# Kernel tuning notes

Measured on AMD Instinct MI355X. Metric: run time of the kernel, lower is better.

The kernel has to match this reference:

```python
import jax, jax.numpy as jnp
import numpy as np

NA = 100000  # number of a-type nodes (rows of adj)
NB = 100000  # number of b-type nodes (cols of adj)
NE = 1600000 # number of edges (nnz of adj)
BF = 128     # b_features
AF = 128     # a_features


def setup_inputs() -> dict:
    key = jax.random.key(0)
    k1, k2, k3, k4, k5, k6 = jax.random.split(key, 6)
    stdv = 1.0 / np.sqrt(BF)
    return {
        "b_input": jax.random.normal(k1, (NB, BF), dtype=jnp.float32),
        "edge_rows": jax.random.randint(k2, (NE,), 0, NA, dtype=jnp.int32),
        "edge_cols": jax.random.randint(k3, (NE,), 0, NB, dtype=jnp.int32),
        "edge_vals": jax.random.uniform(k4, (NE,), dtype=jnp.float32),
        "a_weight": jax.random.uniform(k5, (BF, AF), minval=-stdv, maxval=stdv, dtype=jnp.float32),
        "a_bias": jax.random.uniform(k6, (AF,), minval=-stdv, maxval=stdv, dtype=jnp.float32),
    }


def reference(b_input, edge_rows, edge_cols, edge_vals, a_weight, a_bias):
    # a_support = b_input @ a_weight            : [NB, AF]
    a_support = jnp.matmul(b_input, a_weight)
    # a_output = spmm(adj, a_support)           : [NA, AF]
    # adj[r, c] = edge_vals at (edge_rows, edge_cols)
    gathered = a_support[edge_cols] * edge_vals[:, None]   # [NE, AF]
    a_output = jax.ops.segment_sum(gathered, edge_rows, num_segments=NA)
    # bias=True -> early return of a-side output
    return a_output + a_bias
```

## Files before the change

kernel.cpp:

```cpp
#include <hip/hip_runtime.h>
#include <hip/hip_bf16.h>

#define AF 128
#define BF 128
#define BROWS 32
#define CAP_F 800
#define SORT_CAP 1024
#define CROWS 1024
#define CAP_C 18432
#define CHUNK1 2048
#define NCOARSE_MAX 128

typedef __attribute__((ext_vector_type(8))) short bf16x8;
typedef __attribute__((ext_vector_type(4))) float f32x4;

__device__ inline unsigned short f2bf(float f) {
    unsigned int u = __float_as_uint(f);
    u += 0x7FFF + ((u >> 16) & 1);
    return (unsigned short)(u >> 16);
}
__device__ inline unsigned int pk2bf(float x, float y) {
    __hip_bfloat162 h = __float22bfloat162_rn(make_float2(x, y));
    return *(unsigned int*)&h;
}
__device__ inline float bflo(unsigned int u) { return __uint_as_float(u << 16); }
__device__ inline float bfhi(unsigned int u) { return __uint_as_float(u & 0xFFFF0000u); }

__global__ __launch_bounds__(256) void prep_kernel(const float* __restrict__ W,
                                                   unsigned short* __restrict__ Wt,
                                                   int* __restrict__ grelC,
                                                   int* __restrict__ grelF) {
    const int idx = blockIdx.x * 256 + threadIdx.x;
    const int n = idx >> 7, k = idx & 127;
    Wt[idx] = f2bf(W[(size_t)k * AF + n]);
    if (blockIdx.x == 0) {
        #pragma unroll
        for (int i = threadIdx.x; i < 1024; i += 256) grelC[i] = 0;
        #pragma unroll
        for (int i = threadIdx.x; i < 3328; i += 256) grelF[i] = 0;
    }
}

__global__ __launch_bounds__(256) void gemm_kernel(const float* __restrict__ Bin,
                                                   const unsigned short* __restrict__ Wt,
                                                   unsigned int* __restrict__ Sup, int NB) {
    const int tid = threadIdx.x;
    const int lane = tid & 63;
    const int wave = tid >> 6;
    const int row0 = blockIdx.x * 64;
    const int m = lane & 15;
    const int quad = lane >> 4;

    int arow = row0 + wave * 16 + m;
    int arow_c = (arow < NB) ? arow : (NB - 1);
    const float* ap = Bin + (size_t)arow_c * BF + quad * 8;
    bf16x8 af[4];
    #pragma unroll
    for (int ks = 0; ks < 4; ks++) {
        float4 lo = *(const float4*)(ap + ks * 32);
        float4 hi = *(const float4*)(ap + ks * 32 + 4);
        union { unsigned int u[4]; bf16x8 v; } cv;
        cv.u[0] = pk2bf(lo.x, lo.y); cv.u[1] = pk2bf(lo.z, lo.w);
        cv.u[2] = pk2bf(hi.x, hi.y); cv.u[3] = pk2bf(hi.z, hi.w);
        af[ks] = cv.v;
    }

    f32x4 acc[8];
    #pragma unroll
    for (int nt = 0; nt < 8; nt++) {
        f32x4 a = {0.f, 0.f, 0.f, 0.f};
        const unsigned short* wp = Wt + (size_t)(nt * 16 + m) * 128 + quad * 8;
        #pragma unroll
        for (int ks = 0; ks < 4; ks++) {
            bf16x8 bf = *(const bf16x8*)(wp + ks * 32);
            a = __builtin_amdgcn_mfma_f32_16x16x32_bf16(af[ks], bf, a, 0, 0, 0);
        }
        acc[nt] = a;
    }
    #pragma unroll
    for (int nt = 0; nt < 4; nt++) {
        #pragma unroll
        for (int r = 0; r < 4; r++) {
            int row = row0 + wave * 16 + quad * 4 + r;
            if (row < NB)
                Sup[(size_t)row * 64 + nt * 16 + m] = pk2bf(acc[nt][r], acc[nt + 4][r]);
        }
    }
}

__global__ __launch_bounds__(256) void binA_kernel(const int* __restrict__ rows,
                                                   const int* __restrict__ cols,
                                                   const float* __restrict__ vals,
                                                   int* __restrict__ grelC,
                                                   int2* __restrict__ binnedC,
                                                   int NE, int NCOARSE) {
    __shared__ int h[NCOARSE_MAX];
    __shared__ int rbase[NCOARSE_MAX];
    const int tid = threadIdx.x;
    int base = blockIdx.x * CHUNK1;
    int ke[8]; int px[8]; float pv[8];
    #pragma unroll
    for (int i = 0; i < 8; i++) {
        int e = base + tid + i * 256;
        if (e < NE) {
            int r = rows[e];
            ke[i] = r >> 10;
            px[i] = cols[e] | ((r & 1023) << 17);
            pv[i] = vals[e];
        } else ke[i] = -1;
    }
    if (tid < NCOARSE) h[tid] = 0;
    __syncthreads();
    #pragma unroll
    for (int i = 0; i < 8; i++)
        if (ke[i] >= 0) atomicAdd(&h[ke[i]], 1);
    __syncthreads();
    if (tid < NCOARSE) {
        int c = h[tid];
        rbase[tid] = tid * CAP_C + (c ? atomicAdd(&grelC[tid], c) : 0);
        h[tid] = 0;
    }
    __syncthreads();
    #pragma unroll
    for (int i = 0; i < 8; i++) {
        if (ke[i] >= 0) {
            int lp = atomicAdd(&h[ke[i]], 1);
            binnedC[rbase[ke[i]] + lp] = make_int2(px[i], __float_as_int(pv[i]));
        }
    }
}

__global__ __launch_bounds__(256) void passA2_kernel(const int2* __restrict__ binnedC,
                                                     const int* __restrict__ grelC,
                                                     int* __restrict__ grelF,
                                                     int2* __restrict__ binnedF, int NBUCK) {
    __shared__ int h[32];
    __shared__ int rb[32];
    const int tid = threadIdx.x;
    const int j = blockIdx.x >> 5;
    const int s = blockIdx.x & 31;
    int n = grelC[j]; if (n > CAP_C) n = CAP_C;
    const int st = (n * s) >> 5;
    const int en = (n * (s + 1)) >> 5;
    const int2* src = binnedC + (size_t)j * CAP_C;

    int sub[3]; int qx[3]; int qy[3];
    #pragma unroll
    for (int i = 0; i < 3; i++) {
        int idx = st + tid + i * 256;
        if (idx < en) {
            int2 p = src[idx];
            sub[i] = (p.x >> 22) & 31;
            qx[i] = p.x & 0x3FFFFF;
            qy[i] = p.y;
        } else sub[i] = -1;
    }
    if (tid < 32) h[tid] = 0;
    __syncthreads();
    #pragma unroll
    for (int i = 0; i < 3; i++)
        if (sub[i] >= 0) atomicAdd(&h[sub[i]], 1);
    __syncthreads();
    if (tid < 32) {
        int c = h[tid];
        int fine = j * 32 + tid;
        rb[tid] = (fine < NBUCK) ? (fine * CAP_F + (c ? atomicAdd(&grelF[fine], c) : 0)) : 0;
        h[tid] = 0;
    }
    __syncthreads();
    #pragma unroll
    for (int i = 0; i < 3; i++) {
        if (sub[i] >= 0) {
            int lp = atomicAdd(&h[sub[i]], 1);
            binnedF[(size_t)rb[sub[i]] + lp] = make_int2(qx[i], qy[i]);
        }
    }
}

__global__ __launch_bounds__(256) void spmm_sorted_kernel(const unsigned short* __restrict__ Sup,
                                                          const int2* __restrict__ binned,
                                                          const int* __restrict__ grel,
                                                          const float* __restrict__ bias,
                                                          float* __restrict__ out, int NA) {
    __shared__ int2 spxy[SORT_CAP];
    __shared__ int cnt[BROWS];
    __shared__ int rs[BROWS + 1];
    __shared__ int cur[BROWS];
    const int tid = threadIdx.x;
    const int b = blockIdx.x;
    int n = grel[b]; if (n > CAP_F) n = CAP_F;
    const int2* src = binned + (size_t)b * CAP_F;

    int2 pr[4];
    #pragma unroll
    for (int j = 0; j < 4; j++) {
        int i = tid + j * 256;
        pr[j] = (i < n) ? src[i] : make_int2(-1, 0);
    }
    if (tid < BROWS) cnt[tid] = 0;
    __syncthreads();
    #pragma unroll
    for (int j = 0; j < 4; j++)
        if (pr[j].x >= 0) atomicAdd(&cnt[(pr[j].x >> 17) & 31], 1);
    __syncthreads();
    if (tid < 32) {
        int v = (cnt[tid] + 7) & ~7;
        int x = v;
        #pragma unroll
        for (int off = 1; off < 32; off <<= 1) {
            int t = __shfl_up(x, off);
            if (tid >= off) x += t;
        }
        rs[tid] = x - v;
        cur[tid] = x - v;
        if (tid == 31) rs[32] = x;
    }
    __syncthreads();
    #pragma unroll
    for (int j = 0; j < 4; j++) {
        if (pr[j].x >= 0) {
            int lr = (pr[j].x >> 17) & 31;
            int pos = atomicAdd(&cur[lr], 1);
            spxy[pos] = make_int2(pr[j].x & 0x1FFFF, pr[j].y);
        }
    }
    __syncthreads();
    if (tid < BROWS) {
        int end = rs[tid + 1];
        for (int p = cur[tid]; p < end; p++) spxy[p] = make_int2(0, 0);
    }
    __syncthreads();

    const int lane = tid & 63;
    const int wv = tid >> 6;
    const float b0 = bias[lane];
    const float b1 = bias[64 + lane];
    int r = wv * 8;
    const int rend = r + 8;
    int e = rs[r];
    const int eend = rs[rend];
    int nb = rs[r + 1];
    float ax = 0.f, ay = 0.f;

    int2 q[8]; unsigned int su[8];
    if (e < eend) {
        #pragma unroll
        for (int t = 0; t < 8; t++) q[t] = spxy[e + t];
        #pragma unroll
        for (int t = 0; t < 8; t++)
            su[t] = *(const unsigned int*)(Sup + (size_t)q[t].x * AF + lane * 2);
    }
    while (e < eend) {
        const int en2 = e + 8;
        int2 q2[8]; unsigned int s2[8];
        if (en2 < eend) {
            #pragma unroll
            for (int t = 0; t < 8; t++) q2[t] = spxy[en2 + t];
            #pragma unroll
            for (int t = 0; t < 8; t++)
                s2[t] = *(const unsigned int*)(Sup + (size_t)q2[t].x * AF + lane * 2);
        }
        while (e >= nb) {
            int row = b * BROWS + r;
            if (row < NA) {
                out[(size_t)row * AF + lane]      = ax + b0;
                out[(size_t)row * AF + 64 + lane] = ay + b1;
            }
            ax = 0.f; ay = 0.f;
            ++r; nb = rs[r + 1];
        }
        #pragma unroll
        for (int t = 0; t < 8; t++) {
            float v = __int_as_float(q[t].y);
            ax += v * bflo(su[t]);
            ay += v * bfhi(su[t]);
        }
        #pragma unroll
        for (int t = 0; t < 8; t++) { q[t] = q2[t]; su[t] = s2[t]; }
        e = en2;
    }
    while (r < rend) {
        int row = b * BROWS + r;
        if (row < NA) {
            out[(size_t)row * AF + lane]      = ax + b0;
            out[(size_t)row * AF + 64 + lane] = ay + b1;
        }
        ax = 0.f; ay = 0.f;
        ++r;
    }
}

extern "C" void kernel_launch(void* const* d_in, const int* in_sizes, int n_in,
                              void* d_out, int out_size, void* d_ws, size_t ws_size,
                              hipStream_t stream) {
    const float* b_input   = (const float*)d_in[0];
    const int*   edge_rows = (const int*)d_in[1];
    const int*   edge_cols = (const int*)d_in[2];
    const float* edge_vals = (const float*)d_in[3];
    const float* a_weight  = (const float*)d_in[4];
    const float* a_bias    = (const float*)d_in[5];
    const int NB = in_sizes[0] / BF;
    const int NE = in_sizes[1];
    const int NA = out_size / AF;
    const int NBUCK = (NA + BROWS - 1) / BROWS;
    const int NCOARSE = (NA + CROWS - 1) / CROWS;
    float* out = (float*)d_out;

    char* ws = (char*)d_ws;
    size_t off = 0;
    unsigned short* Sup = (unsigned short*)(ws + off); off += (size_t)NB * AF * sizeof(unsigned short);
    int* grelC = (int*)(ws + off); off += 1024 * sizeof(int);
    int* grelF = (int*)(ws + off); off += 3328 * sizeof(int);
    unsigned short* Wt = (unsigned short*)(ws + off); off += (size_t)128 * 128 * sizeof(unsigned short);
    int2* binnedC = (int2*)(ws + off); off += (size_t)NCOARSE * CAP_C * sizeof(int2);
    int2* binnedF = (int2*)(ws + off); off += (size_t)NBUCK * CAP_F * sizeof(int2);
    (void)ws_size; (void)n_in;

    const int ngemm = (NB + 63) / 64;
    const int npass = (NE + CHUNK1 - 1) / CHUNK1;
    prep_kernel<<<64, 256, 0, stream>>>(a_weight, Wt, grelC, grelF);
    gemm_kernel<<<ngemm, 256, 0, stream>>>(b_input, Wt, (unsigned int*)Sup, NB);
    binA_kernel<<<npass, 256, 0, stream>>>(edge_rows, edge_cols, edge_vals, grelC, binnedC, NE, NCOARSE);
    passA2_kernel<<<NCOARSE * 32, 256, 0, stream>>>(binnedC, grelC, grelF, binnedF, NBUCK);
    spmm_sorted_kernel<<<NBUCK, 256, 0, stream>>>(Sup, binnedF, grelF, a_bias, out, NA);
}
```

Baseline: 236.1 us.

## Merge weight prep, GEMM and coarse binning into one block-partitioned kernel

Replaces three kernel launches (weight transpose, GEMM, coarse edge binning) with a single launch whose first blocks do the GEMM and whose remaining blocks do the binning, so the two independent phases can run concurrently on the GPU. Each GEMM block now transposes and converts the full 128x128 weight to bf16 in LDS itself, instead of reading a precomputed transposed copy from global memory. Counter zeroing moves to a hipMemsetAsync. The cost is redundant per-block weight conversion, about 35 KB of LDS per block that may reduce occupancy for the binning blocks, and an extra memset operation on the stream.

```diff
diff --git a/kernel.cpp b/kernel.cpp
--- a/kernel.cpp
+++ b/kernel.cpp
@@ -26,106 +26,108 @@
 __device__ inline float bflo(unsigned int u) { return __uint_as_float(u << 16); }
 __device__ inline float bfhi(unsigned int u) { return __uint_as_float(u & 0xFFFF0000u); }
 
-__global__ __launch_bounds__(256) void prep_kernel(const float* __restrict__ W,
-                                                   unsigned short* __restrict__ Wt,
-                                                   int* __restrict__ grelC,
-                                                   int* __restrict__ grelF) {
-    const int idx = blockIdx.x * 256 + threadIdx.x;
-    const int n = idx >> 7, k = idx & 127;
-    Wt[idx] = f2bf(W[(size_t)k * AF + n]);
-    if (blockIdx.x == 0) {
-        #pragma unroll
-        for (int i = threadIdx.x; i < 1024; i += 256) grelC[i] = 0;
-        #pragma unroll
-        for (int i = threadIdx.x; i < 3328; i += 256) grelF[i] = 0;
-    }
-}
-
-__global__ __launch_bounds__(256) void gemm_kernel(const float* __restrict__ Bin,
-                                                   const unsigned short* __restrict__ Wt,
-                                                   unsigned int* __restrict__ Sup, int NB) {
-    const int tid = threadIdx.x;
-    const int lane = tid & 63;
-    const int wave = tid >> 6;
-    const int row0 = blockIdx.x * 64;
-    const int m = lane & 15;
-    const int quad = lane >> 4;
-
-    int arow = row0 + wave * 16 + m;
-    int arow_c = (arow < NB) ? arow : (NB - 1);
-    const float* ap = Bin + (size_t)arow_c * BF + quad * 8;
-    bf16x8 af[4];
-    #pragma unroll
-    for (int ks = 0; ks < 4; ks++) {
-        float4 lo = *(const float4*)(ap + ks * 32);
-        float4 hi = *(const float4*)(ap + ks * 32 + 4);
-        union { unsigned int u[4]; bf16x8 v; } cv;
-        cv.u[0] = pk2bf(lo.x, lo.y); cv.u[1] = pk2bf(lo.z, lo.w);
-        cv.u[2] = pk2bf(hi.x, hi.y); cv.u[3] = pk2bf(hi.z, hi.w);
-        af[ks] = cv.v;
-    }
-
-    f32x4 acc[8];
-    #pragma unroll
-    for (int nt = 0; nt < 8; nt++) {
-        f32x4 a = {0.f, 0.f, 0.f, 0.f};
-        const unsigned short* wp = Wt + (size_t)(nt * 16 + m) * 128 + quad * 8;
-        #pragma unroll
-        for (int ks = 0; ks < 4; ks++) {
-            bf16x8 bf = *(const bf16x8*)(wp + ks * 32);
-            a = __builtin_amdgcn_mfma_f32_16x16x32_bf16(af[ks], bf, a, 0, 0, 0);
-        }
-        acc[nt] = a;
-    }
-    #pragma unroll
-    for (int nt = 0; nt < 4; nt++) {
-        #pragma unroll
-        for (int r = 0; r < 4; r++) {
-            int row = row0 + wave * 16 + quad * 4 + r;
-            if (row < NB)
-                Sup[(size_t)row * 64 + nt * 16 + m] = pk2bf(acc[nt][r], acc[nt + 4][r]);
-        }
-    }
-}
-
-__global__ __launch_bounds__(256) void binA_kernel(const int* __restrict__ rows,
-                                                   const int* __restrict__ cols,
-                                                   const float* __restrict__ vals,
-                                                   int* __restrict__ grelC,
-                                                   int2* __restrict__ binnedC,
-                                                   int NE, int NCOARSE) {
+__global__ __launch_bounds__(256) void phase1_kernel(const float* __restrict__ Bin,
+                                                     const float* __restrict__ W,
+                                                     unsigned int* __restrict__ Sup, int NB,
+                                                     const int* __restrict__ rows,
+                                                     const int* __restrict__ cols,
+                                                     const float* __restrict__ vals,
+                                                     int* __restrict__ grelC,
+                                                     int2* __restrict__ binnedC,
+                                                     int NE, int NCOARSE, int ngemm) {
+    __shared__ unsigned short Ws[128][136];
     __shared__ int h[NCOARSE_MAX];
     __shared__ int rbase[NCOARSE_MAX];
     const int tid = threadIdx.x;
-    int base = blockIdx.x * CHUNK1;
-    int ke[8]; int px[8]; float pv[8];
-    #pragma unroll
-    for (int i = 0; i < 8; i++) {
-        int e = base + tid + i * 256;
-        if (e < NE) {
-            int r = rows[e];
-            ke[i] = r >> 10;
-            px[i] = cols[e] | ((r & 1023) << 17);
-            pv[i] = vals[e];
-        } else ke[i] = -1;
-    }
-    if (tid < NCOARSE) h[tid] = 0;
-    __syncthreads();
-    #pragma unroll
-    for (int i = 0; i < 8; i++)
-        if (ke[i] >= 0) atomicAdd(&h[ke[i]], 1);
-    __syncthreads();
-    if (tid < NCOARSE) {
-        int c = h[tid];
-        rbase[tid] = tid * CAP_C + (c ? atomicAdd(&grelC[tid], c) : 0);
-        h[tid] = 0;
-    }
-    __syncthreads();
-    #pragma unroll
-    for (int i = 0; i < 8; i++) {
-        if (ke[i] >= 0) {
-            int lp = atomicAdd(&h[ke[i]], 1);
-            binnedC[rbase[ke[i]] + lp] = make_int2(px[i], __float_as_int(pv[i]));
+
+    if ((int)blockIdx.x < ngemm) {
+        const int lane = tid & 63;
+        const int wave = tid >> 6;
+        const int row0 = blockIdx.x * 64;
+        const int m = lane & 15;
+        const int quad = lane >> 4;
+
+        {
+            int k = tid >> 1;
+            int n0 = (tid & 1) * 64;
+            const float4* src = (const float4*)(W + (size_t)k * AF + n0);
+            #pragma unroll
+            for (int i = 0; i < 16; i++) {
+                float4 v = src[i];
+                int n = n0 + i * 4;
+                Ws[n + 0][k] = f2bf(v.x);
+                Ws[n + 1][k] = f2bf(v.y);
+                Ws[n + 2][k] = f2bf(v.z);
+                Ws[n + 3][k] = f2bf(v.w);
+            }
+        }
+        int arow = row0 + wave * 16 + m;
+        int arow_c = (arow < NB) ? arow : (NB - 1);
+        const float* ap = Bin + (size_t)arow_c * BF + quad * 8;
+        bf16x8 af[4];
+        #pragma unroll
+        for (int ks = 0; ks < 4; ks++) {
+            float4 lo = *(const float4*)(ap + ks * 32);
+            float4 hi = *(const float4*)(ap + ks * 32 + 4);
+            union { unsigned int u[4]; bf16x8 v; } cv;
+            cv.u[0] = pk2bf(lo.x, lo.y); cv.u[1] = pk2bf(lo.z, lo.w);
+            cv.u[2] = pk2bf(hi.x, hi.y); cv.u[3] = pk2bf(hi.z, hi.w);
+            af[ks] = cv.v;
+        }
+        __syncthreads();
+
+        f32x4 acc[8];
+        #pragma unroll
+        for (int nt = 0; nt < 8; nt++) {
+            f32x4 a = {0.f, 0.f, 0.f, 0.f};
+            #pragma unroll
+            for (int ks = 0; ks < 4; ks++) {
+                bf16x8 bf = *(const bf16x8*)(&Ws[nt * 16 + m][ks * 32 + quad * 8]);
+                a = __builtin_amdgcn_mfma_f32_16x16x32_bf16(af[ks], bf, a, 0, 0, 0);
+            }
+            acc[nt] = a;
+        }
+        #pragma unroll
+        for (int nt = 0; nt < 4; nt++) {
+            #pragma unroll
+            for (int r = 0; r < 4; r++) {
+                int row = row0 + wave * 16 + quad * 4 + r;
+                if (row < NB)
+                    Sup[(size_t)row * 64 + nt * 16 + m] = pk2bf(acc[nt][r], acc[nt + 4][r]);
+            }
+        }
+    } else {
+        int bid = blockIdx.x - ngemm;
+        int base = bid * CHUNK1;
+        int ke[8]; int px[8]; float pv[8];
+        #pragma unroll
+        for (int i = 0; i < 8; i++) {
+            int e = base + tid + i * 256;
+            if (e < NE) {
+                int r = rows[e];
+                ke[i] = r >> 10;
+                px[i] = cols[e] | ((r & 1023) << 17);
+                pv[i] = vals[e];
+            } else ke[i] = -1;
+        }
+        if (tid < NCOARSE) h[tid] = 0;
+        __syncthreads();
+        #pragma unroll
+        for (int i = 0; i < 8; i++)
+            if (ke[i] >= 0) atomicAdd(&h[ke[i]], 1);
+        __syncthreads();
+        if (tid < NCOARSE) {
+            int c = h[tid];
+            rbase[tid] = tid * CAP_C + (c ? atomicAdd(&grelC[tid], c) : 0);
+            h[tid] = 0;
+        }
+        __syncthreads();
+        #pragma unroll
+        for (int i = 0; i < 8; i++) {
+            if (ke[i] >= 0) {
+                int lp = atomicAdd(&h[ke[i]], 1);
+                binnedC[rbase[ke[i]] + lp] = make_int2(px[i], __float_as_int(pv[i]));
+            }
         }
     }
 }
@@ -311,16 +313,17 @@
     unsigned short* Sup = (unsigned short*)(ws + off); off += (size_t)NB * AF * sizeof(unsigned short);
     int* grelC = (int*)(ws + off); off += 1024 * sizeof(int);
     int* grelF = (int*)(ws + off); off += 3328 * sizeof(int);
-    unsigned short* Wt = (unsigned short*)(ws + off); off += (size_t)128 * 128 * sizeof(unsigned short);
     int2* binnedC = (int2*)(ws + off); off += (size_t)NCOARSE * CAP_C * sizeof(int2);
     int2* binnedF = (int2*)(ws + off); off += (size_t)NBUCK * CAP_F * sizeof(int2);
     (void)ws_size; (void)n_in;
 
+    hipMemsetAsync(grelC, 0, (1024 + 3328) * sizeof(int), stream);
+
     const int ngemm = (NB + 63) / 64;
     const int npass = (NE + CHUNK1 - 1) / CHUNK1;
-    prep_kernel<<<64, 256, 0, stream>>>(a_weight, Wt, grelC, grelF);
-    gemm_kernel<<<ngemm, 256, 0, stream>>>(b_input, Wt, (unsigned int*)Sup, NB);
-    binA_kernel<<<npass, 256, 0, stream>>>(edge_rows, edge_cols, edge_vals, grelC, binnedC, NE, NCOARSE);
+    phase1_kernel<<<ngemm + npass, 256, 0, stream>>>(
+        b_input, a_weight, (unsigned int*)Sup, NB,
+        edge_rows, edge_cols, edge_vals, grelC, binnedC, NE, NCOARSE, ngemm);
     passA2_kernel<<<NCOARSE * 32, 256, 0, stream>>>(binnedC, grelC, grelF, binnedF, NBUCK);
     spmm_sorted_kernel<<<NBUCK, 256, 0, stream>>>(Sup, binnedF, grelF, a_bias, out, NA);
 }
```

Measured after the change: 220.3 us. 6.7% less time.

## Fuse GEMM and coarse binning into one heterogeneous kernel launch

Applied to the files above, without the earlier changes.

Merges the bf16 MFMA GEMM and the first-level edge binning into a single launch. Block IDs are interleaved so every fifth block does binning and the rest do GEMM tiles, letting the compute-bound and memory/atomic-bound work overlap and removing one launch. The binning chunk per block doubles to 4096 edges, which raises register use for the bin path. Zeroing of the two counter arrays is merged into one loop over the contiguous region.

```diff
diff --git a/kernel.cpp b/kernel.cpp
--- a/kernel.cpp
+++ b/kernel.cpp
@@ -8,7 +8,7 @@
 #define SORT_CAP 1024
 #define CROWS 1024
 #define CAP_C 18432
-#define CHUNK1 2048
+#define CHUNK1 4096
 #define NCOARSE_MAX 128
 
 typedef __attribute__((ext_vector_type(8))) short bf16x8;
@@ -28,104 +28,109 @@
 
 __global__ __launch_bounds__(256) void prep_kernel(const float* __restrict__ W,
                                                    unsigned short* __restrict__ Wt,
-                                                   int* __restrict__ grelC,
-                                                   int* __restrict__ grelF) {
+                                                   int* __restrict__ grels) {
     const int idx = blockIdx.x * 256 + threadIdx.x;
     const int n = idx >> 7, k = idx & 127;
     Wt[idx] = f2bf(W[(size_t)k * AF + n]);
-    if (blockIdx.x == 0) {
-        #pragma unroll
-        for (int i = threadIdx.x; i < 1024; i += 256) grelC[i] = 0;
-        #pragma unroll
-        for (int i = threadIdx.x; i < 3328; i += 256) grelF[i] = 0;
-    }
-}
-
-__global__ __launch_bounds__(256) void gemm_kernel(const float* __restrict__ Bin,
-                                                   const unsigned short* __restrict__ Wt,
-                                                   unsigned int* __restrict__ Sup, int NB) {
-    const int tid = threadIdx.x;
-    const int lane = tid & 63;
-    const int wave = tid >> 6;
-    const int row0 = blockIdx.x * 64;
-    const int m = lane & 15;
-    const int quad = lane >> 4;
-
-    int arow = row0 + wave * 16 + m;
-    int arow_c = (arow < NB) ? arow : (NB - 1);
-    const float* ap = Bin + (size_t)arow_c * BF + quad * 8;
-    bf16x8 af[4];
-    #pragma unroll
-    for (int ks = 0; ks < 4; ks++) {
-        float4 lo = *(const float4*)(ap + ks * 32);
-        float4 hi = *(const float4*)(ap + ks * 32 + 4);
-        union { unsigned int u[4]; bf16x8 v; } cv;
-        cv.u[0] = pk2bf(lo.x, lo.y); cv.u[1] = pk2bf(lo.z, lo.w);
-        cv.u[2] = pk2bf(hi.x, hi.y); cv.u[3] = pk2bf(hi.z, hi.w);
-        af[ks] = cv.v;
-    }
-
-    f32x4 acc[8];
-    #pragma unroll
-    for (int nt = 0; nt < 8; nt++) {
-        f32x4 a = {0.f, 0.f, 0.f, 0.f};
-        const unsigned short* wp = Wt + (size_t)(nt * 16 + m) * 128 + quad * 8;
-        #pragma unroll
-        for (int ks = 0; ks < 4; ks++) {
-            bf16x8 bf = *(const bf16x8*)(wp + ks * 32);
-            a = __builtin_amdgcn_mfma_f32_16x16x32_bf16(af[ks], bf, a, 0, 0, 0);
-        }
-        acc[nt] = a;
-    }
-    #pragma unroll
-    for (int nt = 0; nt < 4; nt++) {
-        #pragma unroll
-        for (int r = 0; r < 4; r++) {
-            int row = row0 + wave * 16 + quad * 4 + r;
-            if (row < NB)
-                Sup[(size_t)row * 64 + nt * 16 + m] = pk2bf(acc[nt][r], acc[nt + 4][r]);
-        }
-    }
-}
-
-__global__ __launch_bounds__(256) void binA_kernel(const int* __restrict__ rows,
-                                                   const int* __restrict__ cols,
-                                                   const float* __restrict__ vals,
-                                                   int* __restrict__ grelC,
-                                                   int2* __restrict__ binnedC,
-                                                   int NE, int NCOARSE) {
+    if (blockIdx.x == 0)
+        for (int i = threadIdx.x; i < 4352; i += 256) grels[i] = 0;
+}
+
+__global__ __launch_bounds__(256) void phase1_kernel(const float* __restrict__ Bin,
+                                                     const unsigned short* __restrict__ Wt,
+                                                     unsigned int* __restrict__ Sup, int NB,
+                                                     const int* __restrict__ rows,
+                                                     const int* __restrict__ cols,
+                                                     const float* __restrict__ vals,
+                                                     int* __restrict__ grelC,
+                                                     int2* __restrict__ binnedC,
+                                                     int NE, int NCOARSE, int ngemm, int nbin) {
     __shared__ int h[NCOARSE_MAX];
     __shared__ int rbase[NCOARSE_MAX];
     const int tid = threadIdx.x;
-    int base = blockIdx.x * CHUNK1;
-    int ke[8]; int px[8]; float pv[8];
-    #pragma unroll
-    for (int i = 0; i < 8; i++) {
-        int e = base + tid + i * 256;
-        if (e < NE) {
-            int r = rows[e];
-            ke[i] = r >> 10;
-            px[i] = cols[e] | ((r & 1023) << 17);
-            pv[i] = vals[e];
-        } else ke[i] = -1;
-    }
-    if (tid < NCOARSE) h[tid] = 0;
-    __syncthreads();
-    #pragma unroll
-    for (int i = 0; i < 8; i++)
-        if (ke[i] >= 0) atomicAdd(&h[ke[i]], 1);
-    __syncthreads();
-    if (tid < NCOARSE) {
-        int c = h[tid];
-        rbase[tid] = tid * CAP_C + (c ? atomicAdd(&grelC[tid], c) : 0);
-        h[tid] = 0;
-    }
-    __syncthreads();
-    #pragma unroll
-    for (int i = 0; i < 8; i++) {
-        if (ke[i] >= 0) {
-            int lp = atomicAdd(&h[ke[i]], 1);
-            binnedC[rbase[ke[i]] + lp] = make_int2(px[i], __float_as_int(pv[i]));
+    const int bid = (int)blockIdx.x;
+
+    bool isbin = false; int id;
+    if ((bid % 5 == 4) && (bid / 5 < nbin)) { isbin = true; id = bid / 5; }
+    else {
+        int g = bid - ((bid / 5 < nbin) ? (bid / 5) : nbin);
+        if (g < ngemm) id = g;
+        else { isbin = true; id = nbin - 1 - (g - ngemm); }
+    }
+
+    if (!isbin) {
+        const int lane = tid & 63;
+        const int wave = tid >> 6;
+        const int row0 = id * 64;
+        const int m = lane & 15;
+        const int quad = lane >> 4;
+
+        int arow = row0 + wave * 16 + m;
+        int arow_c = (arow < NB) ? arow : (NB - 1);
+        const float* ap = Bin + (size_t)arow_c * BF + quad * 8;
+        bf16x8 af[4];
+        #pragma unroll
+        for (int ks = 0; ks < 4; ks++) {
+            float4 lo = *(const float4*)(ap + ks * 32);
+            float4 hi = *(const float4*)(ap + ks * 32 + 4);
+            union { unsigned int u[4]; bf16x8 v; } cv;
+            cv.u[0] = pk2bf(lo.x, lo.y); cv.u[1] = pk2bf(lo.z, lo.w);
+            cv.u[2] = pk2bf(hi.x, hi.y); cv.u[3] = pk2bf(hi.z, hi.w);
+            af[ks] = cv.v;
+        }
+
+        f32x4 acc[8];
+        #pragma unroll
+        for (int nt = 0; nt < 8; nt++) {
+            f32x4 a = {0.f, 0.f, 0.f, 0.f};
+            const unsigned short* wp = Wt + (size_t)(nt * 16 + m) * 128 + quad * 8;
+            #pragma unroll
+            for (int ks = 0; ks < 4; ks++) {
+                bf16x8 bf = *(const bf16x8*)(wp + ks * 32);
+                a = __builtin_amdgcn_mfma_f32_16x16x32_bf16(af[ks], bf, a, 0, 0, 0);
+            }
+            acc[nt] = a;
+        }
+        #pragma unroll
+        for (int nt = 0; nt < 4; nt++) {
+            #pragma unroll
+            for (int r = 0; r < 4; r++) {
+                int row = row0 + wave * 16 + quad * 4 + r;
+                if (row < NB)
+                    Sup[(size_t)row * 64 + nt * 16 + m] = pk2bf(acc[nt][r], acc[nt + 4][r]);
+            }
+        }
+    } else {
+        int base = id * CHUNK1;
+        int ke[16]; int px[16]; float pv[16];
+        #pragma unroll
+        for (int i = 0; i < 16; i++) {
+            int e = base + tid + i * 256;
+            if (e < NE) {
+                int r = rows[e];
+                ke[i] = r >> 10;
+                px[i] = cols[e] | ((r & 1023) << 17);
+                pv[i] = vals[e];
+            } else ke[i] = -1;
+        }
+        if (tid < NCOARSE) h[tid] = 0;
+        __syncthreads();
+        #pragma unroll
+        for (int i = 0; i < 16; i++)
+            if (ke[i] >= 0) atomicAdd(&h[ke[i]], 1);
+        __syncthreads();
+        if (tid < NCOARSE) {
+            int c = h[tid];
+            rbase[tid] = tid * CAP_C + (c ? atomicAdd(&grelC[tid], c) : 0);
+            h[tid] = 0;
+        }
+        __syncthreads();
+        #pragma unroll
+        for (int i = 0; i < 16; i++) {
+            if (ke[i] >= 0) {
+                int lp = atomicAdd(&h[ke[i]], 1);
+                binnedC[rbase[ke[i]] + lp] = make_int2(px[i], __float_as_int(pv[i]));
+            }
         }
     }
 }
@@ -317,10 +322,11 @@
     (void)ws_size; (void)n_in;
 
     const int ngemm = (NB + 63) / 64;
-    const int npass = (NE + CHUNK1 - 1) / CHUNK1;
-    prep_kernel<<<64, 256, 0, stream>>>(a_weight, Wt, grelC, grelF);
-    gemm_kernel<<<ngemm, 256, 0, stream>>>(b_input, Wt, (unsigned int*)Sup, NB);
-    binA_kernel<<<npass, 256, 0, stream>>>(edge_rows, edge_cols, edge_vals, grelC, binnedC, NE, NCOARSE);
+    const int nbin  = (NE + CHUNK1 - 1) / CHUNK1;
+    prep_kernel<<<64, 256, 0, stream>>>(a_weight, Wt, grelC);
+    phase1_kernel<<<ngemm + nbin, 256, 0, stream>>>(
+        b_input, Wt, (unsigned int*)Sup, NB,
+        edge_rows, edge_cols, edge_vals, grelC, binnedC, NE, NCOARSE, ngemm, nbin);
     passA2_kernel<<<NCOARSE * 32, 256, 0, stream>>>(binnedC, grelC, grelF, binnedF, NBUCK);
     spmm_sorted_kernel<<<NBUCK, 256, 0, stream>>>(Sup, binnedF, grelF, a_bias, out, NA);
 }
```

Result: faster. 224.4 us (-5.0%).
